# Kernel optimization log

Measured on AMD Instinct MI355X. Metric: run time of the kernel, lower is better.

Reference implementation:

```python
import jax, jax.numpy as jnp
import numpy as np

N = 100000
E = 1600000
IN_C, HID_C, OUT_C = 512, 128, 40
K = 5
ALPHA = 0.5


def setup_inputs() -> dict:
    key = jax.random.key(0)
    k1, k2, k3, k4, k5, k6 = jax.random.split(key, 6)
    x = jax.random.normal(k1, (N, IN_C), dtype=jnp.float32)
    edge_index = jax.random.randint(k2, (2, E), 0, N, dtype=jnp.int64)
    # lin1: in -> hidden, lin2: hidden -> out (Kaiming-uniform-ish scale)
    W1 = jax.random.normal(k3, (IN_C, HID_C), dtype=jnp.float32) * (1.0 / np.sqrt(IN_C))
    b1 = jax.random.normal(k4, (HID_C,), dtype=jnp.float32) * 0.01
    W2 = jax.random.normal(k5, (HID_C, OUT_C), dtype=jnp.float32) * (1.0 / np.sqrt(HID_C))
    b2 = jax.random.normal(k6, (OUT_C,), dtype=jnp.float32) * 0.01
    return {"x": x, "edge_index": edge_index, "W1": W1, "b1": b1, "W2": W2, "b2": b2}


def _gcn_norm(edge_index, num_nodes):
    # add self-loops with weight 1, then symmetric normalization D^-1/2 A D^-1/2
    loops = jnp.arange(num_nodes, dtype=edge_index.dtype)
    row = jnp.concatenate([edge_index[0], loops])
    col = jnp.concatenate([edge_index[1], loops])
    w = jnp.ones(row.shape[0], dtype=jnp.float32)
    deg = jax.ops.segment_sum(w, col, num_segments=num_nodes)
    dinv = jnp.where(deg > 0, jax.lax.rsqrt(deg), 0.0)
    norm = dinv[row] * w * dinv[col]
    return row, col, norm


def reference(x, edge_index, W1, b1, W2, b2):
    h = x @ W1 + b1                      # [N, HID_C]
    row, col, norm = _gcn_norm(edge_index, N)
    x0 = h
    for _ in range(K):
        # gather source features, scale by edge norm, scatter-add to targets
        agg = jax.ops.segment_sum(norm[:, None] * h[row], col, num_segments=N)
        h = (1.0 - ALPHA) * agg + ALPHA * x0
    return h @ W2 + b2                   # [N, OUT_C]
```

## Files before the change

### kernel.cpp

```cpp
#include <hip/hip_runtime.h>
#include <hip/hip_bf16.h>

#define NN 100000
#define EE 1600000
#define HALFN 50000

typedef __attribute__((ext_vector_type(8))) short short8;
typedef __attribute__((ext_vector_type(4))) float f32x4;

__device__ __forceinline__ short f2bf(float f) {
    __hip_bfloat16 h = __float2bfloat16(f);
    return *reinterpret_cast<short*>(&h);
}
__device__ __forceinline__ float bf2f(unsigned short u) {
    return __uint_as_float((unsigned int)u << 16);
}


__global__ void wct_kernel(const float* __restrict__ W1, const float* __restrict__ W2,
                           const float* __restrict__ b1, short* __restrict__ WcT,
                           float* __restrict__ bc) {
    int t = blockIdx.x * 256 + threadIdx.x;
    if (t < 48 * 512) {
        int j = t >> 9, k = t & 511;
        float s = 0.f;
        if (j < 40)
            for (int i = 0; i < 128; ++i) s = fmaf(W1[k * 128 + i], W2[i * 40 + j], s);
        WcT[j * 512 + k] = f2bf(s);
    } else if (t < 48 * 512 + 48) {
        int j = t - 48 * 512;
        float s = 0.f;
        if (j < 40)
            for (int i = 0; i < 128; ++i) s = fmaf(b1[i], W2[i * 40 + j], s);
        bc[j] = s;
    }
}

__global__ __launch_bounds__(256) void gemm_z0(const float* __restrict__ x,
                                               const short* __restrict__ WcT,
                                               const float* __restrict__ bc,
                                               unsigned short* __restrict__ z0) {
    const int tid = threadIdx.x;
    const int lane = tid & 63;
    const int wave = tid >> 6;
    const int rbase = blockIdx.x * 64 + wave * 16;
    const int row = rbase + (lane & 15);
    const int kc = lane >> 4;
    const bool rok = row < NN;

    f32x4 acc0 = {0.f, 0.f, 0.f, 0.f};
    f32x4 acc1 = {0.f, 0.f, 0.f, 0.f};
    f32x4 acc2 = {0.f, 0.f, 0.f, 0.f};

    const float* xrow = x + (size_t)row * 512 + kc * 8;
    const short* bp0 = WcT + (size_t)(lane & 15) * 512 + kc * 8;
    const short* bp1 = bp0 + 16 * 512;
    const short* bp2 = bp0 + 32 * 512;

    for (int k0 = 0; k0 < 512; k0 += 32) {
        float4 p0 = {0.f, 0.f, 0.f, 0.f}, p1 = {0.f, 0.f, 0.f, 0.f};
        if (rok) {
            p0 = *reinterpret_cast<const float4*>(xrow + k0);
            p1 = *reinterpret_cast<const float4*>(xrow + k0 + 4);
        }
        short8 a;
        a[0] = f2bf(p0.x); a[1] = f2bf(p0.y); a[2] = f2bf(p0.z); a[3] = f2bf(p0.w);
        a[4] = f2bf(p1.x); a[5] = f2bf(p1.y); a[6] = f2bf(p1.z); a[7] = f2bf(p1.w);
        short8 b0 = *reinterpret_cast<const short8*>(bp0 + k0);
        short8 b1 = *reinterpret_cast<const short8*>(bp1 + k0);
        short8 b2 = *reinterpret_cast<const short8*>(bp2 + k0);
        acc0 = __builtin_amdgcn_mfma_f32_16x16x32_bf16(a, b0, acc0, 0, 0, 0);
        acc1 = __builtin_amdgcn_mfma_f32_16x16x32_bf16(a, b1, acc1, 0, 0, 0);
        acc2 = __builtin_amdgcn_mfma_f32_16x16x32_bf16(a, b2, acc2, 0, 0, 0);
    }

    const int cb = lane & 15;
    const int rr = rbase + (lane >> 4) * 4;
#pragma unroll
    for (int q = 0; q < 4; ++q) {
        int r = rr + q;
        if (r < NN) {
            z0[(size_t)r * 64 + cb] = (unsigned short)f2bf(acc0[q] + bc[cb]);
            z0[(size_t)r * 64 + cb + 16] = (unsigned short)f2bf(acc1[q] + bc[cb + 16]);
            z0[(size_t)r * 64 + cb + 32] = (unsigned short)f2bf(acc2[q] + bc[cb + 32]);
        }
    }
}

__global__ void count_kernel(const int* __restrict__ eidx, int* __restrict__ counts) {
    int e = blockIdx.x * 256 + threadIdx.x;
    if (e < EE) atomicAdd(&counts[eidx[EE + e]], 1);
}

__global__ void scan1(const int* __restrict__ counts, int* __restrict__ ptr,
                      int* __restrict__ bsum) {
    __shared__ int s[256];
    int tid = threadIdx.x;
    int i = blockIdx.x * 256 + tid;
    int v = (i < NN) ? counts[i] : 0;
    s[tid] = v;
    __syncthreads();
    for (int off = 1; off < 256; off <<= 1) {
        int t = (tid >= off) ? s[tid - off] : 0;
        __syncthreads();
        s[tid] += t;
        __syncthreads();
    }
    if (i < NN) ptr[i] = s[tid] - v;
    if (tid == 255) bsum[blockIdx.x] = s[255];
}

__global__ void scan2(int* __restrict__ bsum) {
    __shared__ int s[512];
    int tid = threadIdx.x;
    int v = (tid < 391) ? bsum[tid] : 0;
    s[tid] = v;
    __syncthreads();
    for (int off = 1; off < 512; off <<= 1) {
        int t = (tid >= off) ? s[tid - off] : 0;
        __syncthreads();
        s[tid] += t;
        __syncthreads();
    }
    if (tid < 391) bsum[tid] = s[tid] - v;
}

__global__ void scan3(int* __restrict__ ptr, const int* __restrict__ bsum,
                      const int* __restrict__ counts, float* __restrict__ dinvp,
                      int* __restrict__ ptr2) {
    int i = blockIdx.x * 256 + threadIdx.x;
    if (i < NN) {
        int p = ptr[i] + bsum[blockIdx.x];
        ptr[i] = p;
        ptr2[i] = p;
        dinvp[i] = rsqrtf(1.0f + (float)counts[i]);
    }
    if (i == 0) { ptr[NN] = EE; ptr2[NN] = EE; }
}

__global__ void scatter_kernel(const int* __restrict__ eidx,
                               const float* __restrict__ dinvp, int* __restrict__ ptr2,
                               int2* __restrict__ cev) {
    int e = blockIdx.x * 256 + threadIdx.x;
    if (e < EE) {
        int r = eidx[e];
        int c = eidx[EE + e];
        int pos = atomicAdd(&ptr2[c], 1);
        cev[pos] = make_int2(r, __float_as_int(dinvp[r]));
    }
}

__global__ __launch_bounds__(256) void propagate(const unsigned short* __restrict__ zcur,
                                                 const unsigned short* __restrict__ z0q,
                                                 unsigned short* __restrict__ znb,
                                                 float* __restrict__ outf,
                                                 const int* __restrict__ ptr,
                                                 const int2* __restrict__ cev,
                                                 const float* __restrict__ dinvp,
                                                 const float* __restrict__ b2, int last) {
    const int lane = threadIdx.x & 63;
    const int wid = blockIdx.x * 4 + (threadIdx.x >> 6);
    const int n0 = wid, n1 = wid + HALFN;

    int beg0 = __builtin_amdgcn_readfirstlane(ptr[n0]);
    int end0 = __builtin_amdgcn_readfirstlane(ptr[n0 + 1]);
    int beg1 = __builtin_amdgcn_readfirstlane(ptr[n1]);
    int end1 = __builtin_amdgcn_readfirstlane(ptr[n1 + 1]);
    const float dc0 = dinvp[n0], dc1 = dinvp[n1];

    int m0 = end0 - beg0; if (m0 > 64) m0 = 64;
    int m1 = end1 - beg1; if (m1 > 64) m1 = 64;

    int idx0 = beg0 + (lane < m0 ? lane : m0 - 1); if (idx0 < 0) idx0 = 0;
    int idx1 = beg1 + (lane < m1 ? lane : m1 - 1); if (idx1 < 0) idx1 = 0;
    int2 ev0 = cev[idx0];
    int2 ev1 = cev[idx1];
    if (lane >= m0) ev0.y = 0;
    if (lane >= m1) ev1.y = 0;

    const float self0 = bf2f(zcur[(size_t)n0 * 64 + lane]);
    const float self1 = bf2f(zcur[(size_t)n1 * 64 + lane]);
    const float z00 = bf2f(z0q[(size_t)n0 * 64 + lane]);
    const float z01 = bf2f(z0q[(size_t)n1 * 64 + lane]);

    float A0 = dc0 * self0, B0 = 0.f;
    float A1 = dc1 * self1, B1 = 0.f;

    int nc0 = (m0 + 7) >> 3, nc1 = (m1 + 7) >> 3;
    int nc = nc0 > nc1 ? nc0 : nc1;
    for (int c = 0; c < nc; ++c) {
        const int j = c * 8;
        float x[8], y[8];
#pragma unroll
        for (int k = 0; k < 8; ++k) {
            int r0 = __builtin_amdgcn_readlane(ev0.x, j + k);
            int r1 = __builtin_amdgcn_readlane(ev1.x, j + k);
            x[k] = bf2f(zcur[(size_t)r0 * 64 + lane]);
            y[k] = bf2f(zcur[(size_t)r1 * 64 + lane]);
        }
#pragma unroll
        for (int k = 0; k < 8; ++k) {
            float w = __int_as_float(__builtin_amdgcn_readlane(ev0.y, j + k));
            float u = __int_as_float(__builtin_amdgcn_readlane(ev1.y, j + k));
            if (k & 1) { B0 = fmaf(w, x[k], B0); B1 = fmaf(u, y[k], B1); }
            else       { A0 = fmaf(w, x[k], A0); A1 = fmaf(u, y[k], A1); }
        }
    }

    for (int e = beg0 + 64; e < end0; ++e) {
        int2 ee = cev[e];
        A0 = fmaf(__int_as_float(ee.y), bf2f(zcur[(size_t)ee.x * 64 + lane]), A0);
    }
    for (int e = beg1 + 64; e < end1; ++e) {
        int2 ee = cev[e];
        A1 = fmaf(__int_as_float(ee.y), bf2f(zcur[(size_t)ee.x * 64 + lane]), A1);
    }

    float res0 = 0.5f * dc0 * (A0 + B0) + 0.5f * z00;
    float res1 = 0.5f * dc1 * (A1 + B1) + 0.5f * z01;
    if (last) {
        if (lane < 40) {
            outf[(size_t)n0 * 40 + lane] = res0 + b2[lane];
            outf[(size_t)n1 * 40 + lane] = res1 + b2[lane];
        }
    } else {
        znb[(size_t)n0 * 64 + lane] = (unsigned short)f2bf(res0);
        znb[(size_t)n1 * 64 + lane] = (unsigned short)f2bf(res1);
    }
}

extern "C" void kernel_launch(void* const* d_in, const int* in_sizes, int n_in,
                              void* d_out, int out_size, void* d_ws, size_t ws_size,
                              hipStream_t stream) {
    const float* x  = (const float*)d_in[0];
    const int*   ei = (const int*)d_in[1];
    const float* W1 = (const float*)d_in[2];
    const float* b1 = (const float*)d_in[3];
    const float* W2 = (const float*)d_in[4];
    const float* b2 = (const float*)d_in[5];
    float* out = (float*)d_out;

    char* ws = (char*)d_ws;
    short*          WcT  = (short*)(ws + 0);
    float*          bc   = (float*)(ws + 49152);
    unsigned short* z0   = (unsigned short*)(ws + 65536);
    unsigned short* za   = (unsigned short*)(ws + 12865536);
    unsigned short* zb   = (unsigned short*)(ws + 25665536);
    float*          dinv = (float*)(ws + 38465536);
    int*            cnt  = (int*)(ws + 38865536);
    int*            ptr  = (int*)(ws + 39265536);
    int*            bsum = (int*)(ws + 39665664);
    int*            ptr2 = (int*)(ws + 39667712);
    int2*           cev  = (int2*)(ws + 40067840);

    hipMemsetAsync(cnt, 0, NN * sizeof(int), stream);
    wct_kernel<<<97, 256, 0, stream>>>(W1, W2, b1, WcT, bc);
    count_kernel<<<(EE + 255) / 256, 256, 0, stream>>>(ei, cnt);
    scan1<<<391, 256, 0, stream>>>(cnt, ptr, bsum);
    scan2<<<1, 512, 0, stream>>>(bsum);
    scan3<<<391, 256, 0, stream>>>(ptr, bsum, cnt, dinv, ptr2);
    gemm_z0<<<1563, 256, 0, stream>>>(x, WcT, bc, z0);
    scatter_kernel<<<(EE + 255) / 256, 256, 0, stream>>>(ei, dinv, ptr2, cev);

    propagate<<<12500, 256, 0, stream>>>(z0, z0, zb, out, ptr, cev, dinv, b2, 0);
    propagate<<<12500, 256, 0, stream>>>(zb, z0, za, out, ptr, cev, dinv, b2, 0);
    propagate<<<12500, 256, 0, stream>>>(za, z0, zb, out, ptr, cev, dinv, b2, 0);
    propagate<<<12500, 256, 0, stream>>>(zb, z0, za, out, ptr, cev, dinv, b2, 0);
    propagate<<<12500, 256, 0, stream>>>(za, z0, zb, out, ptr, cev, dinv, b2, 1);
}
```

Measured before the change: 426.8 us.

## Restructure propagate: one node per wave, 4 edges in parallel with 8-byte gathers

The propagate kernel now gives each wave one node instead of two. The wave is split into 4 groups of 16 lanes. Each lane gathers 4 bf16 features (8 bytes) per neighbour, so 4 edges are processed at once, and ds_bpermute distributes the edge indices and weights. Partial sums are reduced across groups with xor shuffles. The gemm also zero-fills the padding columns of z0. The change aims to issue fewer, wider memory requests per neighbour row and to stop wasting the 24 padding lanes. In exchange it adds a cross-lane reduction, and per-wave memory-level parallelism drops from two nodes to one.

```diff
diff --git a/kernel.cpp b/kernel.cpp
--- a/kernel.cpp
+++ b/kernel.cpp
@@ -3,17 +3,19 @@
 
 #define NN 100000
 #define EE 1600000
-#define HALFN 50000
 
 typedef __attribute__((ext_vector_type(8))) short short8;
 typedef __attribute__((ext_vector_type(4))) float f32x4;
 
-__device__ __forceinline__ short f2bf(float f) {
+__device__ __forceinline__ unsigned short f2bfu(float f) {
     __hip_bfloat16 h = __float2bfloat16(f);
-    return *reinterpret_cast<short*>(&h);
-}
-__device__ __forceinline__ float bf2f(unsigned short u) {
-    return __uint_as_float((unsigned int)u << 16);
+    return *reinterpret_cast<unsigned short*>(&h);
+}
+__device__ __forceinline__ float bflo(unsigned int u) {
+    return __uint_as_float(u << 16);
+}
+__device__ __forceinline__ float bfhi(unsigned int u) {
+    return __uint_as_float(u & 0xffff0000u);
 }
 
 
@@ -26,7 +28,7 @@
         float s = 0.f;
         if (j < 40)
             for (int i = 0; i < 128; ++i) s = fmaf(W1[k * 128 + i], W2[i * 40 + j], s);
-        WcT[j * 512 + k] = f2bf(s);
+        WcT[j * 512 + k] = (short)f2bfu(s);
     } else if (t < 48 * 512 + 48) {
         int j = t - 48 * 512;
         float s = 0.f;
@@ -64,8 +66,10 @@
             p1 = *reinterpret_cast<const float4*>(xrow + k0 + 4);
         }
         short8 a;
-        a[0] = f2bf(p0.x); a[1] = f2bf(p0.y); a[2] = f2bf(p0.z); a[3] = f2bf(p0.w);
-        a[4] = f2bf(p1.x); a[5] = f2bf(p1.y); a[6] = f2bf(p1.z); a[7] = f2bf(p1.w);
+        a[0] = (short)f2bfu(p0.x); a[1] = (short)f2bfu(p0.y);
+        a[2] = (short)f2bfu(p0.z); a[3] = (short)f2bfu(p0.w);
+        a[4] = (short)f2bfu(p1.x); a[5] = (short)f2bfu(p1.y);
+        a[6] = (short)f2bfu(p1.z); a[7] = (short)f2bfu(p1.w);
         short8 b0 = *reinterpret_cast<const short8*>(bp0 + k0);
         short8 b1 = *reinterpret_cast<const short8*>(bp1 + k0);
         short8 b2 = *reinterpret_cast<const short8*>(bp2 + k0);
@@ -80,9 +84,10 @@
     for (int q = 0; q < 4; ++q) {
         int r = rr + q;
         if (r < NN) {
-            z0[(size_t)r * 64 + cb] = (unsigned short)f2bf(acc0[q] + bc[cb]);
-            z0[(size_t)r * 64 + cb + 16] = (unsigned short)f2bf(acc1[q] + bc[cb + 16]);
-            z0[(size_t)r * 64 + cb + 32] = (unsigned short)f2bf(acc2[q] + bc[cb + 32]);
+            z0[(size_t)r * 64 + cb] = f2bfu(acc0[q] + bc[cb]);
+            z0[(size_t)r * 64 + cb + 16] = f2bfu(acc1[q] + bc[cb + 16]);
+            z0[(size_t)r * 64 + cb + 32] = f2bfu(acc2[q] + bc[cb + 32]);
+            z0[(size_t)r * 64 + cb + 48] = 0;
         }
     }
 }
@@ -159,73 +164,115 @@
                                                  const float* __restrict__ dinvp,
                                                  const float* __restrict__ b2, int last) {
     const int lane = threadIdx.x & 63;
-    const int wid = blockIdx.x * 4 + (threadIdx.x >> 6);
-    const int n0 = wid, n1 = wid + HALFN;
-
-    int beg0 = __builtin_amdgcn_readfirstlane(ptr[n0]);
-    int end0 = __builtin_amdgcn_readfirstlane(ptr[n0 + 1]);
-    int beg1 = __builtin_amdgcn_readfirstlane(ptr[n1]);
-    int end1 = __builtin_amdgcn_readfirstlane(ptr[n1 + 1]);
-    const float dc0 = dinvp[n0], dc1 = dinvp[n1];
-
-    int m0 = end0 - beg0; if (m0 > 64) m0 = 64;
-    int m1 = end1 - beg1; if (m1 > 64) m1 = 64;
-
-    int idx0 = beg0 + (lane < m0 ? lane : m0 - 1); if (idx0 < 0) idx0 = 0;
-    int idx1 = beg1 + (lane < m1 ? lane : m1 - 1); if (idx1 < 0) idx1 = 0;
-    int2 ev0 = cev[idx0];
-    int2 ev1 = cev[idx1];
-    if (lane >= m0) ev0.y = 0;
-    if (lane >= m1) ev1.y = 0;
-
-    const float self0 = bf2f(zcur[(size_t)n0 * 64 + lane]);
-    const float self1 = bf2f(zcur[(size_t)n1 * 64 + lane]);
-    const float z00 = bf2f(z0q[(size_t)n0 * 64 + lane]);
-    const float z01 = bf2f(z0q[(size_t)n1 * 64 + lane]);
-
-    float A0 = dc0 * self0, B0 = 0.f;
-    float A1 = dc1 * self1, B1 = 0.f;
-
-    int nc0 = (m0 + 7) >> 3, nc1 = (m1 + 7) >> 3;
-    int nc = nc0 > nc1 ? nc0 : nc1;
-    for (int c = 0; c < nc; ++c) {
-        const int j = c * 8;
-        float x[8], y[8];
-#pragma unroll
-        for (int k = 0; k < 8; ++k) {
-            int r0 = __builtin_amdgcn_readlane(ev0.x, j + k);
-            int r1 = __builtin_amdgcn_readlane(ev1.x, j + k);
-            x[k] = bf2f(zcur[(size_t)r0 * 64 + lane]);
-            y[k] = bf2f(zcur[(size_t)r1 * 64 + lane]);
-        }
-#pragma unroll
-        for (int k = 0; k < 8; ++k) {
-            float w = __int_as_float(__builtin_amdgcn_readlane(ev0.y, j + k));
-            float u = __int_as_float(__builtin_amdgcn_readlane(ev1.y, j + k));
-            if (k & 1) { B0 = fmaf(w, x[k], B0); B1 = fmaf(u, y[k], B1); }
-            else       { A0 = fmaf(w, x[k], A0); A1 = fmaf(u, y[k], A1); }
-        }
-    }
-
-    for (int e = beg0 + 64; e < end0; ++e) {
-        int2 ee = cev[e];
-        A0 = fmaf(__int_as_float(ee.y), bf2f(zcur[(size_t)ee.x * 64 + lane]), A0);
-    }
-    for (int e = beg1 + 64; e < end1; ++e) {
-        int2 ee = cev[e];
-        A1 = fmaf(__int_as_float(ee.y), bf2f(zcur[(size_t)ee.x * 64 + lane]), A1);
-    }
-
-    float res0 = 0.5f * dc0 * (A0 + B0) + 0.5f * z00;
-    float res1 = 0.5f * dc1 * (A1 + B1) + 0.5f * z01;
+    const int node = blockIdx.x * 4 + (threadIdx.x >> 6);
+    const int t = lane & 15;
+    const int g = lane >> 4;
+    const int t8 = t * 8;
+    const int g4 = g * 4;
+
+    int beg = __builtin_amdgcn_readfirstlane(ptr[node]);
+    int end = __builtin_amdgcn_readfirstlane(ptr[node + 1]);
+    const int deg = end - beg;
+    int m = deg > 64 ? 64 : deg;
+
+    int2 ev = make_int2(0, 0);
+    if (m > 0) ev = cev[beg + (lane < m ? lane : m - 1)];
+    if (lane >= m) ev.y = 0;
+
+    const float dc = dinvp[node];
+    const char* zb = (const char*)zcur;
+
+    uint2 ps = *(const uint2*)(zb + (size_t)node * 128 + t8);
+    float sg = (g == 0) ? dc : 0.0f;
+    float acc0 = sg * bflo(ps.x);
+    float acc1 = sg * bfhi(ps.x);
+    float acc2 = sg * bflo(ps.y);
+    float acc3 = sg * bfhi(ps.y);
+
+    const int nc = (m + 3) >> 2;
+    int c = 0;
+    for (; c + 4 <= nc; c += 4) {
+        int i0 = c * 16 + g4;
+        int r0 = __builtin_amdgcn_ds_bpermute(i0, ev.x);
+        int r1 = __builtin_amdgcn_ds_bpermute(i0 + 16, ev.x);
+        int r2 = __builtin_amdgcn_ds_bpermute(i0 + 32, ev.x);
+        int r3 = __builtin_amdgcn_ds_bpermute(i0 + 48, ev.x);
+        int w0 = __builtin_amdgcn_ds_bpermute(i0, ev.y);
+        int w1 = __builtin_amdgcn_ds_bpermute(i0 + 16, ev.y);
+        int w2 = __builtin_amdgcn_ds_bpermute(i0 + 32, ev.y);
+        int w3 = __builtin_amdgcn_ds_bpermute(i0 + 48, ev.y);
+        uint2 p0 = *(const uint2*)(zb + (size_t)r0 * 128 + t8);
+        uint2 p1 = *(const uint2*)(zb + (size_t)r1 * 128 + t8);
+        uint2 p2 = *(const uint2*)(zb + (size_t)r2 * 128 + t8);
+        uint2 p3 = *(const uint2*)(zb + (size_t)r3 * 128 + t8);
+        float W0 = __int_as_float(w0), W1 = __int_as_float(w1);
+        float W2 = __int_as_float(w2), W3 = __int_as_float(w3);
+        acc0 = fmaf(W0, bflo(p0.x), acc0);
+        acc1 = fmaf(W0, bfhi(p0.x), acc1);
+        acc2 = fmaf(W0, bflo(p0.y), acc2);
+        acc3 = fmaf(W0, bfhi(p0.y), acc3);
+        acc0 = fmaf(W1, bflo(p1.x), acc0);
+        acc1 = fmaf(W1, bfhi(p1.x), acc1);
+        acc2 = fmaf(W1, bflo(p1.y), acc2);
+        acc3 = fmaf(W1, bfhi(p1.y), acc3);
+        acc0 = fmaf(W2, bflo(p2.x), acc0);
+        acc1 = fmaf(W2, bfhi(p2.x), acc1);
+        acc2 = fmaf(W2, bflo(p2.y), acc2);
+        acc3 = fmaf(W2, bfhi(p2.y), acc3);
+        acc0 = fmaf(W3, bflo(p3.x), acc0);
+        acc1 = fmaf(W3, bfhi(p3.x), acc1);
+        acc2 = fmaf(W3, bflo(p3.y), acc2);
+        acc3 = fmaf(W3, bfhi(p3.y), acc3);
+    }
+    for (; c < nc; ++c) {
+        int i0 = c * 16 + g4;
+        int r0 = __builtin_amdgcn_ds_bpermute(i0, ev.x);
+        int w0 = __builtin_amdgcn_ds_bpermute(i0, ev.y);
+        uint2 p0 = *(const uint2*)(zb + (size_t)r0 * 128 + t8);
+        float W0 = __int_as_float(w0);
+        acc0 = fmaf(W0, bflo(p0.x), acc0);
+        acc1 = fmaf(W0, bfhi(p0.x), acc1);
+        acc2 = fmaf(W0, bflo(p0.y), acc2);
+        acc3 = fmaf(W0, bfhi(p0.y), acc3);
+    }
+
+    if (deg > 64) {
+        for (int e2 = beg + 64 + g; e2 < end; e2 += 4) {
+            int2 ee = cev[e2];
+            uint2 p = *(const uint2*)(zb + (size_t)ee.x * 128 + t8);
+            float w = __int_as_float(ee.y);
+            acc0 = fmaf(w, bflo(p.x), acc0);
+            acc1 = fmaf(w, bfhi(p.x), acc1);
+            acc2 = fmaf(w, bflo(p.y), acc2);
+            acc3 = fmaf(w, bfhi(p.y), acc3);
+        }
+    }
+
+    acc0 += __shfl_xor(acc0, 16, 64); acc0 += __shfl_xor(acc0, 32, 64);
+    acc1 += __shfl_xor(acc1, 16, 64); acc1 += __shfl_xor(acc1, 32, 64);
+    acc2 += __shfl_xor(acc2, 16, 64); acc2 += __shfl_xor(acc2, 32, 64);
+    acc3 += __shfl_xor(acc3, 16, 64); acc3 += __shfl_xor(acc3, 32, 64);
+
+    uint2 pz = *(const uint2*)((const char*)z0q + (size_t)node * 128 + t8);
+    float r0v = 0.5f * dc * acc0 + 0.5f * bflo(pz.x);
+    float r1v = 0.5f * dc * acc1 + 0.5f * bfhi(pz.x);
+    float r2v = 0.5f * dc * acc2 + 0.5f * bflo(pz.y);
+    float r3v = 0.5f * dc * acc3 + 0.5f * bfhi(pz.y);
+
     if (last) {
-        if (lane < 40) {
-            outf[(size_t)n0 * 40 + lane] = res0 + b2[lane];
-            outf[(size_t)n1 * 40 + lane] = res1 + b2[lane];
+        if (g == 0 && t < 10) {
+            float4 bv = *(const float4*)(b2 + t * 4);
+            float4 o;
+            o.x = r0v + bv.x; o.y = r1v + bv.y; o.z = r2v + bv.z; o.w = r3v + bv.w;
+            *(float4*)(outf + (size_t)node * 40 + t * 4) = o;
         }
     } else {
-        znb[(size_t)n0 * 64 + lane] = (unsigned short)f2bf(res0);
-        znb[(size_t)n1 * 64 + lane] = (unsigned short)f2bf(res1);
+        if (g == 0) {
+            uint2 s;
+            s.x = ((unsigned int)f2bfu(r1v) << 16) | f2bfu(r0v);
+            s.y = ((unsigned int)f2bfu(r3v) << 16) | f2bfu(r2v);
+            *(uint2*)((char*)znb + (size_t)node * 128 + t8) = s;
+        }
     }
 }
 
@@ -262,9 +309,9 @@
     gemm_z0<<<1563, 256, 0, stream>>>(x, WcT, bc, z0);
     scatter_kernel<<<(EE + 255) / 256, 256, 0, stream>>>(ei, dinv, ptr2, cev);
 
-    propagate<<<12500, 256, 0, stream>>>(z0, z0, zb, out, ptr, cev, dinv, b2, 0);
-    propagate<<<12500, 256, 0, stream>>>(zb, z0, za, out, ptr, cev, dinv, b2, 0);
-    propagate<<<12500, 256, 0, stream>>>(za, z0, zb, out, ptr, cev, dinv, b2, 0);
-    propagate<<<12500, 256, 0, stream>>>(zb, z0, za, out, ptr, cev, dinv, b2, 0);
-    propagate<<<12500, 256, 0, stream>>>(za, z0, zb, out, ptr, cev, dinv, b2, 1);
-}
+    propagate<<<25000, 256, 0, stream>>>(z0, z0, zb, out, ptr, cev, dinv, b2, 0);
+    propagate<<<25000, 256, 0, stream>>>(zb, z0, za, out, ptr, cev, dinv, b2, 0);
+    propagate<<<25000, 256, 0, stream>>>(za, z0, zb, out, ptr, cev, dinv, b2, 0);
+    propagate<<<25000, 256, 0, stream>>>(zb, z0, za, out, ptr, cev, dinv, b2, 0);
+    propagate<<<25000, 256, 0, stream>>>(za, z0, zb, out, ptr, cev, dinv, b2, 1);
+}
```

New measurement: 443.1 us. +3.8%, slower.
